# Optimization experiments

Hardware: AMD Instinct MI355X
Metric: run time of the kernel (lower is better)

## Reference

```python
import jax, jax.numpy as jnp
import numpy as np
import math

NUM_HEADS = 16
HEAD_SIZE = 64
HIDDEN = NUM_HEADS * HEAD_SIZE
LN_EPS = 1e-12


def setup_inputs() -> dict:
    key = jax.random.key(0)
    ks = jax.random.split(key, 8)
    B, Lw, Le, H = 8, 512, 64, HIDDEN
    scale = 0.02
    return {
        "word_hidden_states": jax.random.normal(ks[0], (B, Lw, H), jnp.float32),
        "entity_hidden_states": jax.random.normal(ks[1], (B, Le, H), jnp.float32),
        "attention_mask": jnp.zeros((B, 1, 1, Lw + Le), jnp.float32),
        "Wq": jax.random.normal(ks[2], (H, H), jnp.float32) * scale,
        "bq": jnp.zeros((H,), jnp.float32),
        "Wk": jax.random.normal(ks[3], (H, H), jnp.float32) * scale,
        "bk": jnp.zeros((H,), jnp.float32),
        "Wv": jax.random.normal(ks[4], (H, H), jnp.float32) * scale,
        "bv": jnp.zeros((H,), jnp.float32),
        "Wo": jax.random.normal(ks[5], (H, H), jnp.float32) * scale,
        "bo": jnp.zeros((H,), jnp.float32),
        "ln_w": jnp.ones((H,), jnp.float32),
        "ln_b": jnp.zeros((H,), jnp.float32),
    }


def _layernorm(x, w, b):
    u = jnp.mean(x, axis=-1, keepdims=True)
    s = jnp.mean(jnp.square(x - u), axis=-1, keepdims=True)
    return w * ((x - u) / jnp.sqrt(s + LN_EPS)) + b


def reference(word_hidden_states, entity_hidden_states, attention_mask,
              Wq, bq, Wk, bk, Wv, bv, Wo, bo, ln_w, ln_b):
    B, Lw, H = word_hidden_states.shape
    x = jnp.concatenate([word_hidden_states, entity_hidden_states], axis=1)  # [B,S,H]
    S = x.shape[1]

    def heads(t):  # [B,S,H] -> [B,nh,S,hd]
        return t.reshape(B, S, NUM_HEADS, HEAD_SIZE).transpose(0, 2, 1, 3)

    q = heads(x @ Wq + bq)
    k = heads(x @ Wk + bk)
    v = heads(x @ Wv + bv)

    scores = jnp.einsum("bhqd,bhkd->bhqk", q, k) / math.sqrt(HEAD_SIZE)
    scores = scores + attention_mask  # additive mask, broadcast [B,1,1,S]
    probs = jax.nn.softmax(scores, axis=-1)
    ctx = jnp.einsum("bhqk,bhkd->bhqd", probs, v)
    ctx = ctx.transpose(0, 2, 1, 3).reshape(B, S, H)

    # SelfOutput (shared weights) applied per-stream; equivalent on concat since
    # residual is the concatenated input and LayerNorm is per-token.
    out = _layernorm(ctx @ Wo + bo + x, ln_w, ln_b)
    return out[:, :Lw, :], out[:, Lw:, :]
```

## Files before the change

### kernel.cpp

```cpp
#include <hip/hip_runtime.h>

#define NHEADS 16
#define HDIM   64
#define HID    1024
#define BATCH  8
#define LW     512
#define LE     64
#define SEQ    576
#define MTOT   (BATCH * SEQ)

typedef unsigned short u16;
typedef __bf16 bf16x8 __attribute__((ext_vector_type(8)));
typedef float  f32x4  __attribute__((ext_vector_type(4)));

__device__ __forceinline__ u16 f2bf(float f) {
  union { float f; unsigned int i; } x;
  x.f = f;
  unsigned int u = x.i;
  unsigned int r = (u + 0x7FFFu + ((u >> 16) & 1u)) >> 16;
  return (u16)r;
}
__device__ __forceinline__ unsigned int pk2(float a, float b) {
  return (unsigned int)f2bf(a) | ((unsigned int)f2bf(b) << 16);
}

__device__ __forceinline__ void gload16(const u16* g, u16* l) {
  __builtin_amdgcn_global_load_lds(
      (const __attribute__((address_space(1))) void*)g,
      (__attribute__((address_space(3))) void*)l, 16, 0, 0);
}

__global__ __launch_bounds__(256) void prep_k(
    const float* __restrict__ w0, const float* __restrict__ w1,
    const float* __restrict__ w2, const float* __restrict__ w3,
    u16* __restrict__ wt,
    const float* __restrict__ word, const float* __restrict__ ent,
    u16* __restrict__ xb)
{
  const int bid = blockIdx.x, tid = threadIdx.x;
  if (bid < 4096) {
    __shared__ u16 tile[32][33];
    const int z = bid >> 10, rem = bid & 1023;
    const int bx = rem & 31, by = rem >> 5;
    const float* src = (z == 0) ? w0 : (z == 1) ? w1 : (z == 2) ? w2 : w3;
    u16* dst = wt + (size_t)z * HID * HID;
    const int tx = tid & 31, ty = tid >> 5;
    const int nx = bx * 32, ky = by * 32;
#pragma unroll
    for (int j = 0; j < 4; ++j)
      tile[ty * 4 + j][tx] = f2bf(src[(size_t)(ky + ty * 4 + j) * HID + nx + tx]);
    __syncthreads();
#pragma unroll
    for (int j = 0; j < 4; ++j)
      dst[(size_t)(nx + ty * 4 + j) * HID + ky + tx] = tile[tx][ty * 4 + j];
  } else {
    const int row = bid - 4096;
    const int bb = row / SEQ, ss = row - bb * SEQ;
    const float* src = (ss < LW) ? word + (size_t)(bb * LW + ss) * HID
                                 : ent  + (size_t)(bb * LE + (ss - LW)) * HID;
    float4 v = *(const float4*)(src + tid * 4);
    ushort4 o;
    o.x = f2bf(v.x); o.y = f2bf(v.y); o.z = f2bf(v.z); o.w = f2bf(v.w);
    *(ushort4*)(xb + (size_t)row * HID + tid * 4) = o;
  }
}

__global__ __launch_bounds__(256) void qkv_gemm_k(
    const u16* __restrict__ xb, const u16* __restrict__ wt,
    const float* __restrict__ bq, const float* __restrict__ bk, const float* __restrict__ bv,
    u16* __restrict__ q_ws, u16* __restrict__ k_ws, u16* __restrict__ v_ws)
{
  __shared__ u16 sh[4 * 64 * 68];
  const int which = blockIdx.z;
  const u16* W = wt + (size_t)which * HID * HID;
  const float* bias = (which == 0) ? bq : (which == 1) ? bk : bv;
  const int m0 = blockIdx.x * 128, n0 = blockIdx.y * 128;
  const int tid = threadIdx.x, lane = tid & 63, wv = tid >> 6;
  const int lr = lane & 15, quad = lane >> 4;
  const int wm = (wv >> 1) * 64, wn = (wv & 1) * 64;

  const int subrow = lane >> 3;
  const int gsw = ((lane & 7) ^ subrow) * 8;
  const int fsw = lr & 7;

  u16* As = sh;
  u16* Bs = sh + 8192;

  const f32x4 fz = {0.f, 0.f, 0.f, 0.f};
  f32x4 acc[4][4];
#pragma unroll
  for (int a = 0; a < 4; ++a)
#pragma unroll
    for (int b = 0; b < 4; ++b) acc[a][b] = fz;

  for (int ki = 0; ki < 16; ++ki) {
    const int k0 = ki * 64;
#pragma unroll
    for (int j = 0; j < 4; ++j) {
      int row = (wv * 4 + j) * 8 + subrow;
      u16* ldst = sh + ((wv * 4 + j) * 64 + lane) * 8;
      gload16(xb + (size_t)(m0 + row) * HID + k0 + gsw, ldst);
      gload16(W  + (size_t)(n0 + row) * HID + k0 + gsw, ldst + 8192);
    }
    __syncthreads();
#pragma unroll
    for (int ks = 0; ks < 2; ++ks) {
      bf16x8 af[4], bfr[4];
#pragma unroll
      for (int i = 0; i < 4; ++i) {
        af[i]  = *(const bf16x8*)(&As[(wm + i * 16 + lr) * 64 + (((ks * 4 + quad) ^ fsw) * 8)]);
        bfr[i] = *(const bf16x8*)(&Bs[(wn + i * 16 + lr) * 64 + (((ks * 4 + quad) ^ fsw) * 8)]);
      }
      if (which < 2) {
#pragma unroll
        for (int a = 0; a < 4; ++a)
#pragma unroll
          for (int b = 0; b < 4; ++b)
            acc[a][b] = __builtin_amdgcn_mfma_f32_16x16x32_bf16(bfr[a], af[b], acc[a][b], 0, 0, 0);
      } else {
#pragma unroll
        for (int a = 0; a < 4; ++a)
#pragma unroll
          for (int b = 0; b < 4; ++b)
            acc[a][b] = __builtin_amdgcn_mfma_f32_16x16x32_bf16(af[a], bfr[b], acc[a][b], 0, 0, 0);
      }
    }
    __syncthreads();
  }

  u16* tb = sh + wv * (64 * 68);
  const int head = (n0 + wn) >> 6;
  const int mbase = m0 + wm;
  const int bb = mbase / SEQ;
  const int ssb = mbase - bb * SEQ;

  if (which < 2) {
    float4 bias4[4];
#pragma unroll
    for (int ni = 0; ni < 4; ++ni)
      bias4[ni] = *(const float4*)(bias + n0 + wn + ni * 16 + quad * 4);
#pragma unroll
    for (int mi = 0; mi < 4; ++mi)
#pragma unroll
      for (int ni = 0; ni < 4; ++ni) {
        uint2 w2v;
        w2v.x = pk2(acc[ni][mi][0] + bias4[ni].x, acc[ni][mi][1] + bias4[ni].y);
        w2v.y = pk2(acc[ni][mi][2] + bias4[ni].z, acc[ni][mi][3] + bias4[ni].w);
        *(uint2*)(&tb[(mi * 16 + lr) * 68 + ni * 16 + quad * 4]) = w2v;
      }
    u16* drow = (which == 0 ? q_ws : k_ws)
              + ((size_t)(bb * NHEADS + head) * SEQ + ssb) * HDIM;
#pragma unroll
    for (int i = 0; i < 8; ++i) {
      int rrow = i * 8 + (lane >> 3);
      int seg = lane & 7;
      bf16x8 v8 = *(const bf16x8*)(&tb[rrow * 68 + seg * 8]);
      *(bf16x8*)(drow + (size_t)rrow * HDIM + seg * 8) = v8;
    }
  } else {
    float bcol[4];
#pragma unroll
    for (int ni = 0; ni < 4; ++ni) bcol[ni] = bias[n0 + wn + ni * 16 + lr];
#pragma unroll
    for (int mi = 0; mi < 4; ++mi)
#pragma unroll
      for (int ni = 0; ni < 4; ++ni) {
        uint2 w2v;
        w2v.x = pk2(acc[mi][ni][0] + bcol[ni], acc[mi][ni][1] + bcol[ni]);
        w2v.y = pk2(acc[mi][ni][2] + bcol[ni], acc[mi][ni][3] + bcol[ni]);
        *(uint2*)(&tb[(ni * 16 + lr) * 68 + (mi >> 1) * 32 + quad * 8 + (mi & 1) * 4]) = w2v;
      }
    u16* dcol = v_ws + ((size_t)(bb * NHEADS + head) * HDIM) * SEQ + ssb;
#pragma unroll
    for (int i = 0; i < 8; ++i) {
      int d = i * 8 + (lane >> 3);
      int seg = lane & 7;
      bf16x8 v8 = *(const bf16x8*)(&tb[d * 68 + seg * 8]);
      *(bf16x8*)(dcol + (size_t)d * SEQ + seg * 8) = v8;
    }
  }
}

__global__ __launch_bounds__(256) void attn_k(
    const u16* __restrict__ q_ws, const u16* __restrict__ k_ws,
    const u16* __restrict__ v_ws, const float* __restrict__ mask,
    u16* __restrict__ ctxh)
{
  __shared__ u16 Ks[4096];
  __shared__ u16 Vs[4096];
  __shared__ float ms[576];
  const int bhx = blockIdx.x, qt = blockIdx.y;
  const int b = bhx >> 4, h = bhx & 15;
  const int tid = threadIdx.x, lane = tid & 63, wv = tid >> 6;
  const int lr = lane & 15, quad = lane >> 4;
  const int q0 = qt * 64 + wv * 16;
  const u16* kbh = k_ws + (size_t)bhx * SEQ * HDIM;
  const u16* vbh = v_ws + (size_t)bhx * HDIM * SEQ;
  const u16* qp  = q_ws + ((size_t)bhx * SEQ + q0) * HDIM;
  const float* mrow = mask + b * SEQ;

  if (tid < 144) *(float4*)(&ms[tid * 4]) = *(const float4*)(mrow + tid * 4);

  const int subrow = lane >> 3;
  const int gsw = (lane & 7) ^ subrow;

  bf16x8 qf[2];
  qf[0] = *(const bf16x8*)(qp + lr * HDIM + quad * 8);
  qf[1] = *(const bf16x8*)(qp + lr * HDIM + 32 + quad * 8);

  const f32x4 fz = {0.f, 0.f, 0.f, 0.f};
  f32x4 oa[4] = {fz, fz, fz, fz};
  f32x4 rsv = fz;
  const int fA = lr & 7;

  for (int ci = 0; ci < 9; ++ci) {
    const int c = ci * 64;
#pragma unroll
    for (int j = 0; j < 2; ++j) {
      int row = (wv * 2 + j) * 8 + subrow;
      gload16(kbh + ((size_t)(c + row)) * HDIM + gsw * 8,
              &Ks[((wv * 2 + j) * 64 + lane) * 8]);
      gload16(vbh + (size_t)row * SEQ + c + gsw * 8,
              &Vs[((wv * 2 + j) * 64 + lane) * 8]);
    }
    __syncthreads();
    f32x4 s[4] = {fz, fz, fz, fz};
#pragma unroll
    for (int ks = 0; ks < 2; ++ks)
#pragma unroll
      for (int t = 0; t < 4; ++t) {
        bf16x8 kf = *(const bf16x8*)(&Ks[(t * 16 + lr) * 64 + (((ks * 4 + quad) ^ fA) * 8)]);
        s[t] = __builtin_amdgcn_mfma_f32_16x16x32_bf16(kf, qf[ks], s[t], 0, 0, 0);
      }
    unsigned int pk0[4], pk1[4];
#pragma unroll
    for (int t = 0; t < 4; ++t) {
      float4 mv = *(const float4*)(&ms[c + t * 16 + quad * 4]);
      s[t][0] = __expf(s[t][0] * 0.125f + mv.x);
      s[t][1] = __expf(s[t][1] * 0.125f + mv.y);
      s[t][2] = __expf(s[t][2] * 0.125f + mv.z);
      s[t][3] = __expf(s[t][3] * 0.125f + mv.w);
      rsv += s[t];
      pk0[t] = pk2(s[t][0], s[t][1]);
      pk1[t] = pk2(s[t][2], s[t][3]);
    }
#pragma unroll
    for (int ks = 0; ks < 2; ++ks) {
      union { unsigned int u[4]; bf16x8 v; } ap;
      ap.u[0] = pk0[ks * 2];     ap.u[1] = pk1[ks * 2];
      ap.u[2] = pk0[ks * 2 + 1]; ap.u[3] = pk1[ks * 2 + 1];
#pragma unroll
      for (int n = 0; n < 4; ++n) {
        bf16x8 vf = *(const bf16x8*)(&Vs[(n * 16 + lr) * 64 + (((ks * 4 + quad) ^ fA) * 8)]);
        oa[n] = __builtin_amdgcn_mfma_f32_16x16x32_bf16(ap.v, vf, oa[n], 0, 0, 0);
      }
    }
    __syncthreads();
  }

  float rl = rsv[0] + rsv[1] + rsv[2] + rsv[3];
  rl += __shfl_xor(rl, 16);
  rl += __shfl_xor(rl, 32);
  float inv = 1.0f / rl;
  float invr[4];
#pragma unroll
  for (int r = 0; r < 4; ++r) invr[r] = __shfl(inv, quad * 4 + r);

  u16* pw = (wv < 2) ? &Ks[wv * 2048] : &Vs[(wv - 2) * 2048];
#pragma unroll
  for (int n = 0; n < 4; ++n)
#pragma unroll
    for (int r = 0; r < 4; ++r)
      pw[(quad * 4 + r) * 68 + n * 16 + lr] = f2bf(oa[n][r] * invr[r]);
  const int token0 = b * SEQ + q0;
  u16* cb = ctxh + ((size_t)h * MTOT + token0) * HDIM;
#pragma unroll
  for (int i = 0; i < 2; ++i) {
    int row = lane & 15;
    int seg = (lane >> 4) + i * 4;
    bf16x8 v8 = *(const bf16x8*)(&pw[row * 68 + seg * 8]);
    *(bf16x8*)(cb + (size_t)row * HDIM + seg * 8) = v8;
  }
}

__global__ __launch_bounds__(256) void out_gemm_k(
    const u16* __restrict__ ctxh, const u16* __restrict__ wto,
    const float* __restrict__ bo,
    const float* __restrict__ word, const float* __restrict__ ent,
    float* __restrict__ y)
{
  __shared__ u16 sh[10240];
  u16* As = sh;
  u16* Bs = sh + 2048;
  const int m0 = blockIdx.x * 32, n0 = blockIdx.y * 128;
  const int tid = threadIdx.x, lane = tid & 63, wv = tid >> 6;
  const int lr = lane & 15, quad = lane >> 4;
  const int wn = wv * 32;
  const int subrow = lane >> 3;
  const int gsw = ((lane & 7) ^ subrow) * 8;
  const int fsw = lr & 7;

  const f32x4 fz = {0.f, 0.f, 0.f, 0.f};
  f32x4 acc[2][2];
#pragma unroll
  for (int mi = 0; mi < 2; ++mi)
#pragma unroll
    for (int ni = 0; ni < 2; ++ni) acc[mi][ni] = fz;

  for (int hb = 0; hb < 16; ++hb) {
    {
      int row = wv * 8 + subrow;
      gload16(ctxh + ((size_t)hb * MTOT + (m0 + row)) * HDIM + gsw,
              As + (wv * 64 + lane) * 8);
    }
#pragma unroll
    for (int j = 0; j < 4; ++j) {
      int row = (wv * 4 + j) * 8 + subrow;
      gload16(wto + (size_t)(n0 + row) * HID + hb * 64 + gsw,
              Bs + ((wv * 4 + j) * 64 + lane) * 8);
    }
    __syncthreads();
#pragma unroll
    for (int ks = 0; ks < 2; ++ks) {
      const int kc = (((ks * 4 + quad) ^ fsw) * 8);
      bf16x8 af[2], bfr[2];
#pragma unroll
      for (int i = 0; i < 2; ++i) {
        af[i]  = *(const bf16x8*)(&As[(i * 16 + lr) * 64 + kc]);
        bfr[i] = *(const bf16x8*)(&Bs[(wn + i * 16 + lr) * 64 + kc]);
      }
#pragma unroll
      for (int mi = 0; mi < 2; ++mi)
#pragma unroll
        for (int ni = 0; ni < 2; ++ni)
          acc[mi][ni] = __builtin_amdgcn_mfma_f32_16x16x32_bf16(af[mi], bfr[ni], acc[mi][ni], 0, 0, 0);
    }
    __syncthreads();
  }

#pragma unroll
  for (int mi = 0; mi < 2; ++mi) {
    int rowb = m0 + mi * 16 + quad * 4;
#pragma unroll
    for (int r = 0; r < 4; ++r) {
      int row = rowb + r;
      int bb = row / SEQ, ss = row - bb * SEQ;
      const float* res = (ss < LW) ? (word + (size_t)(bb * LW + ss) * HID)
                                   : (ent  + (size_t)(bb * LE + (ss - LW)) * HID);
#pragma unroll
      for (int ni = 0; ni < 2; ++ni) {
        int col = n0 + wn + ni * 16 + lr;
        y[(size_t)row * HID + col] = acc[mi][ni][r] + bo[col] + res[col];
      }
    }
  }
}

__global__ __launch_bounds__(256) void ln_k(
    const float* __restrict__ y, const float* __restrict__ lnw,
    const float* __restrict__ lnb, float* __restrict__ out)
{
  const int row = blockIdx.x;
  const int tid = threadIdx.x;
  __shared__ float ssum[4], sqq[4];

  const float* yr = y + (size_t)row * HID;
  float4 v = *(const float4*)(yr + tid * 4);
  float s = v.x + v.y + v.z + v.w;
  float q = v.x * v.x + v.y * v.y + v.z * v.z + v.w * v.w;
#pragma unroll
  for (int o = 32; o > 0; o >>= 1) { s += __shfl_xor(s, o); q += __shfl_xor(q, o); }
  if ((tid & 63) == 0) { ssum[tid >> 6] = s; sqq[tid >> 6] = q; }
  __syncthreads();
  s = ssum[0] + ssum[1] + ssum[2] + ssum[3];
  q = sqq[0] + sqq[1] + sqq[2] + sqq[3];
  float mean = s * (1.0f / HID);
  float var  = q * (1.0f / HID) - mean * mean;
  float rstd = rsqrtf(var + 1e-12f);

  int bb = row / SEQ, ss2 = row - bb * SEQ;
  float* dst = (ss2 < LW)
             ? out + (size_t)(bb * LW + ss2) * HID
             : out + (size_t)BATCH * LW * HID + (size_t)(bb * LE + (ss2 - LW)) * HID;

  float4 w4 = *(const float4*)(lnw + tid * 4);
  float4 b4 = *(const float4*)(lnb + tid * 4);
  float4 o4;
  o4.x = w4.x * (v.x - mean) * rstd + b4.x;
  o4.y = w4.y * (v.y - mean) * rstd + b4.y;
  o4.z = w4.z * (v.z - mean) * rstd + b4.z;
  o4.w = w4.w * (v.w - mean) * rstd + b4.w;
  *(float4*)(dst + tid * 4) = o4;
}

extern "C" void kernel_launch(void* const* d_in, const int* in_sizes, int n_in,
                              void* d_out, int out_size, void* d_ws, size_t ws_size,
                              hipStream_t stream) {
  const float* word = (const float*)d_in[0];
  const float* ent  = (const float*)d_in[1];
  const float* mask = (const float*)d_in[2];
  const float* Wq   = (const float*)d_in[3];
  const float* bq   = (const float*)d_in[4];
  const float* Wk   = (const float*)d_in[5];
  const float* bk   = (const float*)d_in[6];
  const float* Wv   = (const float*)d_in[7];
  const float* bv   = (const float*)d_in[8];
  const float* Wo   = (const float*)d_in[9];
  const float* bo   = (const float*)d_in[10];
  const float* lnw  = (const float*)d_in[11];
  const float* lnb  = (const float*)d_in[12];

  char* base = (char*)d_ws;
  u16*   wt   = (u16*)base;
  u16*   q_ws = (u16*)(base + (size_t)8 * 1024 * 1024);
  u16*   k_ws = q_ws + (size_t)MTOT * HID;
  u16*   v_ws = k_ws + (size_t)MTOT * HID;
  u16*   ctxh = v_ws + (size_t)MTOT * HID;
  char*  xy   = (char*)(ctxh + (size_t)MTOT * HID);
  u16*   xb   = (u16*)xy;
  float* y    = (float*)xy;

  hipLaunchKernelGGL(prep_k, dim3(4096 + MTOT), dim3(256), 0, stream,
                     Wq, Wk, Wv, Wo, wt, word, ent, xb);
  hipLaunchKernelGGL(qkv_gemm_k, dim3(MTOT / 128, HID / 128, 3), dim3(256), 0, stream,
                     xb, wt, bq, bk, bv, q_ws, k_ws, v_ws);
  hipLaunchKernelGGL(attn_k, dim3(BATCH * NHEADS, SEQ / 64), dim3(256), 0, stream,
                     q_ws, k_ws, v_ws, mask, ctxh);
  hipLaunchKernelGGL(out_gemm_k, dim3(MTOT / 32, HID / 128), dim3(256), 0, stream,
                     ctxh, wt + (size_t)3 * HID * HID, bo, word, ent, y);
  hipLaunchKernelGGL(ln_k, dim3(MTOT), dim3(256), 0, stream,
                     y, lnw, lnb, (float*)d_out);
}
```

Baseline: 197.2 us.

## Pipeline QKV GEMM with double-buffered LDS and widen prep/LN kernels

The QKV GEMM now uses a 256x128 tile with 512 threads and double-buffered LDS. Global loads for upcoming k-steps are issued ahead, with explicit waitcnt, barriers and priority hints, so memory traffic overlaps with MFMA work. The prep kernel now transposes 64x64 weight tiles using vectorized loads and stores and converts four rows per block. LayerNorm handles one row per wavefront, which removes the shared-memory reduction and block sync. The hand-tuned waitcnt counts and the larger LDS footprint carry correctness and occupancy risk.

Measured after the change: 197.1 us. Within noise of the previous version (-0.0%).

```diff
diff --git a/kernel.cpp b/kernel.cpp
--- a/kernel.cpp
+++ b/kernel.cpp
@@ -38,53 +38,185 @@
     u16* __restrict__ xb)
 {
   const int bid = blockIdx.x, tid = threadIdx.x;
-  if (bid < 4096) {
-    __shared__ u16 tile[32][33];
-    const int z = bid >> 10, rem = bid & 1023;
-    const int bx = rem & 31, by = rem >> 5;
+  if (bid < 1024) {
+    __shared__ u16 tile[64][65];
+    const int z = bid >> 8, rem = bid & 255;
+    const int bx = rem & 15, by = rem >> 4;
     const float* src = (z == 0) ? w0 : (z == 1) ? w1 : (z == 2) ? w2 : w3;
     u16* dst = wt + (size_t)z * HID * HID;
-    const int tx = tid & 31, ty = tid >> 5;
-    const int nx = bx * 32, ky = by * 32;
-#pragma unroll
-    for (int j = 0; j < 4; ++j)
-      tile[ty * 4 + j][tx] = f2bf(src[(size_t)(ky + ty * 4 + j) * HID + nx + tx]);
+    const int nx = bx * 64, ky = by * 64;
+    const int lrow = tid >> 4;
+    const int lcol = (tid & 15) * 4;
+#pragma unroll
+    for (int j = 0; j < 4; ++j) {
+      const int kk = lrow + j * 16;
+      float4 v = *(const float4*)(src + (size_t)(ky + kk) * HID + nx + lcol);
+      tile[kk][lcol + 0] = f2bf(v.x);
+      tile[kk][lcol + 1] = f2bf(v.y);
+      tile[kk][lcol + 2] = f2bf(v.z);
+      tile[kk][lcol + 3] = f2bf(v.w);
+    }
     __syncthreads();
-#pragma unroll
-    for (int j = 0; j < 4; ++j)
-      dst[(size_t)(nx + ty * 4 + j) * HID + ky + tx] = tile[tx][ty * 4 + j];
+    const int orow = tid >> 2;
+    const int oseg = (tid & 3) * 16;
+    union { u16 u[16]; bf16x8 v[2]; } tt;
+#pragma unroll
+    for (int i = 0; i < 16; ++i) tt.u[i] = tile[oseg + i][orow];
+    u16* dp = dst + (size_t)(nx + orow) * HID + ky + oseg;
+    *(bf16x8*)(dp) = tt.v[0];
+    *(bf16x8*)(dp + 8) = tt.v[1];
   } else {
-    const int row = bid - 4096;
+    const int row = (bid - 1024) * 4 + (tid >> 6);
+    const int lane = tid & 63;
     const int bb = row / SEQ, ss = row - bb * SEQ;
     const float* src = (ss < LW) ? word + (size_t)(bb * LW + ss) * HID
                                  : ent  + (size_t)(bb * LE + (ss - LW)) * HID;
-    float4 v = *(const float4*)(src + tid * 4);
-    ushort4 o;
-    o.x = f2bf(v.x); o.y = f2bf(v.y); o.z = f2bf(v.z); o.w = f2bf(v.w);
-    *(ushort4*)(xb + (size_t)row * HID + tid * 4) = o;
-  }
-}
-
-__global__ __launch_bounds__(256) void qkv_gemm_k(
+    u16* drow = xb + (size_t)row * HID;
+#pragma unroll
+    for (int i = 0; i < 4; ++i) {
+      const int f = i * 256 + lane * 4;
+      float4 v = *(const float4*)(src + f);
+      ushort4 o;
+      o.x = f2bf(v.x); o.y = f2bf(v.y); o.z = f2bf(v.z); o.w = f2bf(v.w);
+      *(ushort4*)(drow + f) = o;
+    }
+  }
+}
+
+#define MFMA_L(AF, BL)                                                        \
+  if (which < 2) {                                                            \
+    _Pragma("unroll")                                                         \
+    for (int mi = 0; mi < 4; ++mi)                                            \
+      _Pragma("unroll")                                                       \
+      for (int nj = 0; nj < 2; ++nj)                                          \
+        _Pragma("unroll")                                                     \
+        for (int ks = 0; ks < 2; ++ks)                                        \
+          acc[nj][mi] = __builtin_amdgcn_mfma_f32_16x16x32_bf16(              \
+              BL[nj][ks], AF[mi][ks], acc[nj][mi], 0, 0, 0);                  \
+  } else {                                                                    \
+    _Pragma("unroll")                                                         \
+    for (int mi = 0; mi < 4; ++mi)                                            \
+      _Pragma("unroll")                                                       \
+      for (int nj = 0; nj < 2; ++nj)                                          \
+        _Pragma("unroll")                                                     \
+        for (int ks = 0; ks < 2; ++ks)                                        \
+          acc[mi][nj] = __builtin_amdgcn_mfma_f32_16x16x32_bf16(              \
+              AF[mi][ks], BL[nj][ks], acc[mi][nj], 0, 0, 0);                  \
+  }
+
+#define MFMA_R(AF, BH)                                                        \
+  if (which < 2) {                                                            \
+    _Pragma("unroll")                                                         \
+    for (int mi = 0; mi < 4; ++mi)                                            \
+      _Pragma("unroll")                                                       \
+      for (int nj = 0; nj < 2; ++nj)                                          \
+        _Pragma("unroll")                                                     \
+        for (int ks = 0; ks < 2; ++ks)                                        \
+          acc[2 + nj][mi] = __builtin_amdgcn_mfma_f32_16x16x32_bf16(          \
+              BH[nj][ks], AF[mi][ks], acc[2 + nj][mi], 0, 0, 0);              \
+  } else {                                                                    \
+    _Pragma("unroll")                                                         \
+    for (int mi = 0; mi < 4; ++mi)                                            \
+      _Pragma("unroll")                                                       \
+      for (int nj = 0; nj < 2; ++nj)                                          \
+        _Pragma("unroll")                                                     \
+        for (int ks = 0; ks < 2; ++ks)                                        \
+          acc[mi][2 + nj] = __builtin_amdgcn_mfma_f32_16x16x32_bf16(          \
+              AF[mi][ks], BH[nj][ks], acc[mi][2 + nj], 0, 0, 0);              \
+  }
+
+#define QSTEP(S, CA, CL, NA, NL)                                              \
+  {                                                                           \
+    const int s_ = (S);                                                       \
+    const int bo_ = (s_ & 1) * 24576;                                         \
+    u16* As_ = sh + bo_;                                                      \
+    u16* Bs_ = As_ + 16384;                                                   \
+    u16* Ao_ = sh + (24576 - bo_);                                            \
+    u16* Bo_ = Ao_ + 16384;                                                   \
+                                                           \
+    _Pragma("unroll")                                                         \
+    for (int nj = 0; nj < 2; ++nj) {                                          \
+      bH[nj][0] = *(const bf16x8*)(&Bs_[(wn + (2 + nj) * 16 + lr) * 64 + k0o]); \
+      bH[nj][1] = *(const bf16x8*)(&Bs_[(wn + (2 + nj) * 16 + lr) * 64 + k1o]); \
+    }                                                                         \
+    if (s_ < 15) {                                                            \
+      gload16(bsrc + (size_t)0 * 64 * HID + (s_ + 1) * 64, Bo_ + 0 * 4096 + ldst); \
+      gload16(bsrc + (size_t)1 * 64 * HID + (s_ + 1) * 64, Bo_ + 1 * 4096 + ldst); \
+    }                                                                         \
+    asm volatile("s_waitcnt lgkmcnt(4)" ::: "memory");                        \
+    __builtin_amdgcn_sched_barrier(0);                                        \
+    __builtin_amdgcn_s_setprio(1);                                            \
+    MFMA_L(CA, CL)                                                            \
+    __builtin_amdgcn_s_setprio(0);                                            \
+    __builtin_amdgcn_s_barrier();                                             \
+                                                           \
+    if (s_ < 14) {                                                            \
+      gload16(asrc + (size_t)0 * 64 * HID + (s_ + 2) * 64, As_ + 0 * 4096 + ldst); \
+      gload16(asrc + (size_t)1 * 64 * HID + (s_ + 2) * 64, As_ + 1 * 4096 + ldst); \
+      gload16(asrc + (size_t)2 * 64 * HID + (s_ + 2) * 64, As_ + 2 * 4096 + ldst); \
+      gload16(asrc + (size_t)3 * 64 * HID + (s_ + 2) * 64, As_ + 3 * 4096 + ldst); \
+      asm volatile("s_waitcnt vmcnt(4)" ::: "memory");                        \
+    } else {                                                                  \
+      asm volatile("s_waitcnt vmcnt(0)" ::: "memory");                        \
+    }                                                                         \
+    __builtin_amdgcn_s_barrier();                                             \
+    if (s_ < 15) {                                                            \
+      _Pragma("unroll")                                                       \
+      for (int mi = 0; mi < 4; ++mi) {                                        \
+        NA[mi][0] = *(const bf16x8*)(&Ao_[(wm + mi * 16 + lr) * 64 + k0o]);   \
+        NA[mi][1] = *(const bf16x8*)(&Ao_[(wm + mi * 16 + lr) * 64 + k1o]);   \
+      }                                                                       \
+      _Pragma("unroll")                                                       \
+      for (int nj = 0; nj < 2; ++nj) {                                        \
+        NL[nj][0] = *(const bf16x8*)(&Bo_[(wn + nj * 16 + lr) * 64 + k0o]);   \
+        NL[nj][1] = *(const bf16x8*)(&Bo_[(wn + nj * 16 + lr) * 64 + k1o]);   \
+      }                                                                       \
+      asm volatile("s_waitcnt lgkmcnt(12)" ::: "memory");                     \
+    } else {                                                                  \
+      asm volatile("s_waitcnt lgkmcnt(0)" ::: "memory");                      \
+    }                                                                         \
+    __builtin_amdgcn_sched_barrier(0);                                        \
+    __builtin_amdgcn_s_setprio(1);                                            \
+    MFMA_R(CA, bH)                                                            \
+    __builtin_amdgcn_s_setprio(0);                                            \
+    __builtin_amdgcn_s_barrier();                                             \
+  }
+
+__global__ __launch_bounds__(512, 2) void qkv_gemm_k(
     const u16* __restrict__ xb, const u16* __restrict__ wt,
     const float* __restrict__ bq, const float* __restrict__ bk, const float* __restrict__ bv,
     u16* __restrict__ q_ws, u16* __restrict__ k_ws, u16* __restrict__ v_ws)
 {
-  __shared__ u16 sh[4 * 64 * 68];
+  __shared__ u16 sh[49152];
   const int which = blockIdx.z;
   const u16* W = wt + (size_t)which * HID * HID;
   const float* bias = (which == 0) ? bq : (which == 1) ? bk : bv;
-  const int m0 = blockIdx.x * 128, n0 = blockIdx.y * 128;
+  const int m0 = blockIdx.x * 256, n0 = blockIdx.y * 128;
   const int tid = threadIdx.x, lane = tid & 63, wv = tid >> 6;
   const int lr = lane & 15, quad = lane >> 4;
   const int wm = (wv >> 1) * 64, wn = (wv & 1) * 64;
-
-  const int subrow = lane >> 3;
-  const int gsw = ((lane & 7) ^ subrow) * 8;
   const int fsw = lr & 7;
-
-  u16* As = sh;
-  u16* Bs = sh + 8192;
+  const int k0o = (quad ^ fsw) * 8;
+  const int k1o = ((4 + quad) ^ fsw) * 8;
+
+  const int srow = tid >> 3;
+  const int goff = ((tid & 7) ^ (srow & 7)) * 8;
+  const u16* asrc = xb + (size_t)(m0 + srow) * HID + goff;
+  const u16* bsrc = W  + (size_t)(n0 + srow) * HID + goff;
+  const int ldst = tid * 8;
+
+  gload16(asrc + (size_t)0 * 64 * HID, sh + 0 * 4096 + ldst);
+  gload16(asrc + (size_t)1 * 64 * HID, sh + 1 * 4096 + ldst);
+  gload16(asrc + (size_t)2 * 64 * HID, sh + 2 * 4096 + ldst);
+  gload16(asrc + (size_t)3 * 64 * HID, sh + 3 * 4096 + ldst);
+  gload16(bsrc + (size_t)0 * 64 * HID, sh + 16384 + 0 * 4096 + ldst);
+  gload16(bsrc + (size_t)1 * 64 * HID, sh + 16384 + 1 * 4096 + ldst);
+  gload16(asrc + (size_t)0 * 64 * HID + 64, sh + 24576 + 0 * 4096 + ldst);
+  gload16(asrc + (size_t)1 * 64 * HID + 64, sh + 24576 + 1 * 4096 + ldst);
+  gload16(asrc + (size_t)2 * 64 * HID + 64, sh + 24576 + 2 * 4096 + ldst);
+  gload16(asrc + (size_t)3 * 64 * HID + 64, sh + 24576 + 3 * 4096 + ldst);
+  asm volatile("s_waitcnt vmcnt(4)" ::: "memory");
+  __builtin_amdgcn_s_barrier();
 
   const f32x4 fz = {0.f, 0.f, 0.f, 0.f};
   f32x4 acc[4][4];
@@ -93,39 +225,22 @@
 #pragma unroll
     for (int b = 0; b < 4; ++b) acc[a][b] = fz;
 
-  for (int ki = 0; ki < 16; ++ki) {
-    const int k0 = ki * 64;
-#pragma unroll
-    for (int j = 0; j < 4; ++j) {
-      int row = (wv * 4 + j) * 8 + subrow;
-      u16* ldst = sh + ((wv * 4 + j) * 64 + lane) * 8;
-      gload16(xb + (size_t)(m0 + row) * HID + k0 + gsw, ldst);
-      gload16(W  + (size_t)(n0 + row) * HID + k0 + gsw, ldst + 8192);
-    }
-    __syncthreads();
-#pragma unroll
-    for (int ks = 0; ks < 2; ++ks) {
-      bf16x8 af[4], bfr[4];
-#pragma unroll
-      for (int i = 0; i < 4; ++i) {
-        af[i]  = *(const bf16x8*)(&As[(wm + i * 16 + lr) * 64 + (((ks * 4 + quad) ^ fsw) * 8)]);
-        bfr[i] = *(const bf16x8*)(&Bs[(wn + i * 16 + lr) * 64 + (((ks * 4 + quad) ^ fsw) * 8)]);
-      }
-      if (which < 2) {
-#pragma unroll
-        for (int a = 0; a < 4; ++a)
-#pragma unroll
-          for (int b = 0; b < 4; ++b)
-            acc[a][b] = __builtin_amdgcn_mfma_f32_16x16x32_bf16(bfr[a], af[b], acc[a][b], 0, 0, 0);
-      } else {
-#pragma unroll
-        for (int a = 0; a < 4; ++a)
-#pragma unroll
-          for (int b = 0; b < 4; ++b)
-            acc[a][b] = __builtin_amdgcn_mfma_f32_16x16x32_bf16(af[a], bfr[b], acc[a][b], 0, 0, 0);
-      }
-    }
-    __syncthreads();
+  bf16x8 afA[4][2], afB[4][2], bLA[2][2], bLB[2][2], bH[2][2];
+
+#pragma unroll
+  for (int mi = 0; mi < 4; ++mi) {
+    afA[mi][0] = *(const bf16x8*)(&sh[(wm + mi * 16 + lr) * 64 + k0o]);
+    afA[mi][1] = *(const bf16x8*)(&sh[(wm + mi * 16 + lr) * 64 + k1o]);
+  }
+#pragma unroll
+  for (int nj = 0; nj < 2; ++nj) {
+    bLA[nj][0] = *(const bf16x8*)(&sh[16384 + (wn + nj * 16 + lr) * 64 + k0o]);
+    bLA[nj][1] = *(const bf16x8*)(&sh[16384 + (wn + nj * 16 + lr) * 64 + k1o]);
+  }
+
+  for (int s2 = 0; s2 < 16; s2 += 2) {
+    QSTEP(s2,     afA, bLA, afB, bLB)
+    QSTEP(s2 + 1, afB, bLB, afA, bLA)
   }
 
   u16* tb = sh + wv * (64 * 68);
@@ -360,20 +475,21 @@
     const float* __restrict__ y, const float* __restrict__ lnw,
     const float* __restrict__ lnb, float* __restrict__ out)
 {
-  const int row = blockIdx.x;
   const int tid = threadIdx.x;
-  __shared__ float ssum[4], sqq[4];
+  const int row = blockIdx.x * 4 + (tid >> 6);
+  const int lane = tid & 63;
 
   const float* yr = y + (size_t)row * HID;
-  float4 v = *(const float4*)(yr + tid * 4);
-  float s = v.x + v.y + v.z + v.w;
-  float q = v.x * v.x + v.y * v.y + v.z * v.z + v.w * v.w;
+  float4 v[4];
+  float s = 0.f, q = 0.f;
+#pragma unroll
+  for (int i = 0; i < 4; ++i) {
+    v[i] = *(const float4*)(yr + i * 256 + lane * 4);
+    s += v[i].x + v[i].y + v[i].z + v[i].w;
+    q += v[i].x * v[i].x + v[i].y * v[i].y + v[i].z * v[i].z + v[i].w * v[i].w;
+  }
 #pragma unroll
   for (int o = 32; o > 0; o >>= 1) { s += __shfl_xor(s, o); q += __shfl_xor(q, o); }
-  if ((tid & 63) == 0) { ssum[tid >> 6] = s; sqq[tid >> 6] = q; }
-  __syncthreads();
-  s = ssum[0] + ssum[1] + ssum[2] + ssum[3];
-  q = sqq[0] + sqq[1] + sqq[2] + sqq[3];
   float mean = s * (1.0f / HID);
   float var  = q * (1.0f / HID) - mean * mean;
   float rstd = rsqrtf(var + 1e-12f);
@@ -383,14 +499,18 @@
              ? out + (size_t)(bb * LW + ss2) * HID
              : out + (size_t)BATCH * LW * HID + (size_t)(bb * LE + (ss2 - LW)) * HID;
 
-  float4 w4 = *(const float4*)(lnw + tid * 4);
-  float4 b4 = *(const float4*)(lnb + tid * 4);
-  float4 o4;
-  o4.x = w4.x * (v.x - mean) * rstd + b4.x;
-  o4.y = w4.y * (v.y - mean) * rstd + b4.y;
-  o4.z = w4.z * (v.z - mean) * rstd + b4.z;
-  o4.w = w4.w * (v.w - mean) * rstd + b4.w;
-  *(float4*)(dst + tid * 4) = o4;
+#pragma unroll
+  for (int i = 0; i < 4; ++i) {
+    const int f = i * 256 + lane * 4;
+    float4 w4 = *(const float4*)(lnw + f);
+    float4 b4 = *(const float4*)(lnb + f);
+    float4 o4;
+    o4.x = w4.x * (v[i].x - mean) * rstd + b4.x;
+    o4.y = w4.y * (v[i].y - mean) * rstd + b4.y;
+    o4.z = w4.z * (v[i].z - mean) * rstd + b4.z;
+    o4.w = w4.w * (v[i].w - mean) * rstd + b4.w;
+    *(float4*)(dst + f) = o4;
+  }
 }
 
 extern "C" void kernel_launch(void* const* d_in, const int* in_sizes, int n_in,
@@ -420,14 +540,14 @@
   u16*   xb   = (u16*)xy;
   float* y    = (float*)xy;
 
-  hipLaunchKernelGGL(prep_k, dim3(4096 + MTOT), dim3(256), 0, stream,
+  hipLaunchKernelGGL(prep_k, dim3(1024 + MTOT / 4), dim3(256), 0, stream,
                      Wq, Wk, Wv, Wo, wt, word, ent, xb);
-  hipLaunchKernelGGL(qkv_gemm_k, dim3(MTOT / 128, HID / 128, 3), dim3(256), 0, stream,
+  hipLaunchKernelGGL(qkv_gemm_k, dim3(MTOT / 256, HID / 128, 3), dim3(512), 0, stream,
                      xb, wt, bq, bk, bv, q_ws, k_ws, v_ws);
   hipLaunchKernelGGL(attn_k, dim3(BATCH * NHEADS, SEQ / 64), dim3(256), 0, stream,
                      q_ws, k_ws, v_ws, mask, ctxh);
   hipLaunchKernelGGL(out_gemm_k, dim3(MTOT / 32, HID / 128), dim3(256), 0, stream,
                      ctxh, wt + (size_t)3 * HID * HID, bo, word, ent, y);
-  hipLaunchKernelGGL(ln_k, dim3(MTOT), dim3(256), 0, stream,
+  hipLaunchKernelGGL(ln_k, dim3(MTOT / 4), dim3(256), 0, stream,
                      y, lnw, lnb, (float*)d_out);
 }
```
